# Kernel tuning notes

Hardware: AMD Instinct MI355X
Metric: run time of the kernel (lower is better)

## Reference

```python
import jax, jax.numpy as jnp
import numpy as np

N_USERS = 100000   # n
N_ITEMS = 50000    # m
N_EDGES = 1000000  # observed user-item interactions
D = 64             # embedding dim
ALPHA = 1.0        # Rankformer alpha
CLAMP = 1e-6       # args.rankformer_clamp_value (min clamp on omega norm)


def setup_inputs() -> dict:
    key = jax.random.key(0)
    k1, k2, k3 = jax.random.split(key, 3)
    x = jax.random.normal(k1, (N_USERS + N_ITEMS, D), dtype=jnp.float32)
    u = jax.random.randint(k2, (N_EDGES,), 0, N_USERS, dtype=jnp.int64)
    i = jax.random.randint(k3, (N_EDGES,), 0, N_ITEMS, dtype=jnp.int64)
    return {"x": x, "u": u, "i": i}


def reference(x, u, i):
    seg = jax.ops.segment_sum
    n, m = N_USERS, N_ITEMS
    dt = x.dtype

    # degree of each user; duj = number of non-interacted items
    dui = seg(jnp.ones((u.shape[0],), dt), u, num_segments=n)
    duj = m - dui
    dui = jnp.maximum(dui, 1.0)[:, None]  # [n,1]
    duj = jnp.maximum(duj, 1.0)[:, None]  # [n,1]

    # F.normalize(x): row-wise L2 with eps=1e-12
    xn = x / jnp.maximum(jnp.linalg.norm(x, axis=1, keepdims=True), 1e-12)
    xu, xi = xn[:n], xn[n:]   # normalized user / item features
    vu, vi = x[:n], x[n:]     # raw (value) user / item features

    xi_e = xi[i]              # [E,d] gathered item features per edge
    vi_e = vi[i]
    xui = jnp.sum(xu[u] * xi_e, axis=1, keepdims=True)  # [E,1] edge scores

    sxi = seg(xi_e, u, num_segments=n)          # sum of pos-item x per user
    sxj = jnp.sum(xi, axis=0) - sxi             # rest (neg) sum
    svi = seg(vi_e, u, num_segments=n)
    svj = jnp.sum(vi, axis=0) - svi

    b_pos = jnp.sum(xu * sxi, axis=1, keepdims=True) / dui
    b_neg = jnp.sum(xu * sxj, axis=1, keepdims=True) / duj

    du1 = jnp.sum(xu * sxi, axis=1, keepdims=True) / dui - b_neg + ALPHA
    du2 = -jnp.sum(xu * sxj, axis=1, keepdims=True) / duj + b_pos + ALPHA

    di1 = (jnp.sum(xi * seg((xu / dui)[u], i, num_segments=m), axis=1, keepdims=True)
           + seg(((-b_neg + ALPHA) / dui)[u], i, num_segments=m))
    rest_x = jnp.sum(xu / duj, axis=0)[None, :] - seg((xu / duj)[u], i, num_segments=m)
    rest_b = (jnp.sum((b_pos + ALPHA) / duj, axis=0)[None, :]
              - seg(((b_pos + ALPHA) / duj)[u], i, num_segments=m))
    di2 = -jnp.sum(xi * rest_x, axis=1, keepdims=True) + rest_b

    A = seg(xui * vi_e, u, num_segments=n)      # [n,d]
    # xvi.sum(0): S[a,b] = sum_m vi[m,a]*xi[m,b]  (never materialize [m,d,d])
    S = jnp.einsum('ma,mb->ab', vi, xi)
    zu1 = A / dui - svi * (b_neg - ALPHA) / dui
    zu2 = (xu @ S - A) / duj - svj * (b_pos + ALPHA) / duj

    zi1 = (seg(xui * vu[u] / dui[u], i, num_segments=m)
           - seg((vu * (b_neg - ALPHA) / dui)[u], i, num_segments=m))
    # ((xu/duj) outer vu).sum(0): T[a,b] = sum_n (xu/duj)[n,a]*vu[n,b]
    T = jnp.einsum('na,nb->ab', xu / duj, vu)
    rest_v = (jnp.sum(vu * (b_pos + ALPHA) / duj, axis=0)[None, :]
              - seg((vu * (b_pos + ALPHA) / duj)[u], i, num_segments=m))
    zi2 = xi @ T - seg(xui * (vu / duj)[u], i, num_segments=m) - rest_v

    z = jnp.concatenate([zu1 + zu2, zi1 + zi2], axis=0)          # [n+m,d]
    d1 = jnp.maximum(jnp.concatenate([du1, di1], axis=0), CLAMP)  # [n+m,1]
    d2 = jnp.maximum(jnp.concatenate([du2, di2], axis=0), CLAMP)
    return z / (d1 + d2)
```

## Files before the change

kernel.cpp:

```cpp
#include <hip/hip_runtime.h>

#define NU 100000
#define NI 50000
#define DD 64
#define ALPHA_C 1.0f
#define EPS_CLAMP 1e-6f

__device__ __forceinline__ float rsum16(float v) {
  v += __shfl_xor(v, 1, 64);
  v += __shfl_xor(v, 2, 64);
  v += __shfl_xor(v, 4, 64);
  v += __shfl_xor(v, 8, 64);
  return v;
}
__device__ __forceinline__ float xgrp2(float v) {
  v += __shfl_xor(v, 16, 64);
  v += __shfl_xor(v, 32, 64);
  return v;
}
__device__ __forceinline__ float wsum(float v) { return xgrp2(rsum16(v)); }

__global__ void k_norm_sums(const float* __restrict__ x, float* __restrict__ inv_norm,
                            float* __restrict__ sum_xi, float* __restrict__ sum_vi) {
  __shared__ float sx_s[DD], sv_s[DD];
  if (threadIdx.x < DD) { sx_s[threadIdx.x] = 0.f; sv_s[threadIdx.x] = 0.f; }
  __syncthreads();
  int lane = threadIdx.x & 63;
  int g = lane >> 4, c = lane & 15;
  int wid = blockIdx.x * 4 + (threadIdx.x >> 6);
  int nw  = gridDim.x * 4;
  float sx0=0,sx1=0,sx2=0,sx3=0, sv0=0,sv1=0,sv2=0,sv3=0;
  for (int rb = wid * 4; rb < NU + NI; rb += nw * 4) {
    int r = rb + g;
    const float4 v4 = *(const float4*)(x + (size_t)r * DD + 4 * c);
    float p = v4.x*v4.x + v4.y*v4.y + v4.z*v4.z + v4.w*v4.w;
    p = rsum16(p);
    float inv = 1.0f / fmaxf(sqrtf(p), 1e-12f);
    if (c == 0) inv_norm[r] = inv;
    float fi = (r >= NU) ? 1.f : 0.f;
    float fx = fi * inv;
    sv0 += fi*v4.x; sv1 += fi*v4.y; sv2 += fi*v4.z; sv3 += fi*v4.w;
    sx0 += fx*v4.x; sx1 += fx*v4.y; sx2 += fx*v4.z; sx3 += fx*v4.w;
  }
  atomicAdd(&sx_s[4*c+0], sx0); atomicAdd(&sx_s[4*c+1], sx1);
  atomicAdd(&sx_s[4*c+2], sx2); atomicAdd(&sx_s[4*c+3], sx3);
  atomicAdd(&sv_s[4*c+0], sv0); atomicAdd(&sv_s[4*c+1], sv1);
  atomicAdd(&sv_s[4*c+2], sv2); atomicAdd(&sv_s[4*c+3], sv3);
  __syncthreads();
  if (threadIdx.x < DD) {
    atomicAdd(&sum_xi[threadIdx.x], sx_s[threadIdx.x]);
    atomicAdd(&sum_vi[threadIdx.x], sv_s[threadIdx.x]);
  }
}

__global__ void k_count2(const int* __restrict__ u, const int* __restrict__ it,
                         int* __restrict__ du, int* __restrict__ di,
                         int* __restrict__ ru_, int* __restrict__ ri_, int E) {
  int t = blockIdx.x * blockDim.x + threadIdx.x;
  int stride = gridDim.x * blockDim.x;
  for (int e = t; e < E; e += stride) {
    ru_[e] = atomicAdd(&du[u[e]], 1);
    ri_[e] = atomicAdd(&di[it[e]], 1);
  }
}

__global__ void k_scan2(const int* __restrict__ cnt0, int n0, int* __restrict__ off0,
                        const int* __restrict__ cnt1, int n1, int* __restrict__ off1) {
  const int* cnt = blockIdx.x ? cnt1 : cnt0;
  int n          = blockIdx.x ? n1   : n0;
  int* off       = blockIdx.x ? off1 : off0;
  __shared__ int wsum_s[16];
  __shared__ int carry_s;
  int t = threadIdx.x, lane = t & 63, wv = t >> 6;
  if (t == 0) carry_s = 0;
  __syncthreads();
  for (int base = 0; base < n; base += 1024 * 8) {
    int v[8];
    int s = 0;
    int i0 = base + t * 8;
#pragma unroll
    for (int k = 0; k < 8; ++k) {
      int idx = i0 + k;
      v[k] = (idx < n) ? cnt[idx] : 0;
      s += v[k];
    }
    int incl = s;
#pragma unroll
    for (int d = 1; d < 64; d <<= 1) {
      int t2 = __shfl_up(incl, d, 64);
      if (lane >= d) incl += t2;
    }
    if (lane == 63) wsum_s[wv] = incl;
    __syncthreads();
    int woff = 0, total = 0;
#pragma unroll
    for (int w = 0; w < 16; ++w) {
      int ws_v = wsum_s[w];
      woff += (w < wv) ? ws_v : 0;
      total += ws_v;
    }
    int excl = carry_s + woff + incl - s;
#pragma unroll
    for (int k = 0; k < 8; ++k) {
      int idx = i0 + k;
      if (idx < n) off[idx] = excl;
      excl += v[k];
    }
    __syncthreads();
    if (t == 0) carry_s += total;
    __syncthreads();
  }
  if (t == 0) off[n] = carry_s;
}

__global__ void k_scatter3(const int* __restrict__ u, const int* __restrict__ it,
                           const int* __restrict__ ru_, const int* __restrict__ ri_,
                           const int* __restrict__ uoff, const int* __restrict__ ioff, int E,
                           int* __restrict__ uev, unsigned long long* __restrict__ iue) {
  int t = blockIdx.x * blockDim.x + threadIdx.x;
  int stride = gridDim.x * blockDim.x;
  for (int e = t; e < E; e += stride) {
    int uu = u[e], ii = it[e];
    int pu = uoff[uu] + ru_[e];
    int pi = ioff[ii] + ri_[e];
    __builtin_nontemporal_store(ii, &uev[pu]);
    unsigned long long packed = (unsigned long long)(unsigned)uu |
                                ((unsigned long long)(unsigned)pu << 32);
    __builtin_nontemporal_store(packed, &iue[pi]);
  }
}

#define GRID_OUT 256
#define GS_OUT 85
#define OCH 32
__global__ void k_outer4(const float* __restrict__ x, const float* __restrict__ inv_norm,
                         const int* __restrict__ du, float* __restrict__ part) {
  __shared__ float rows_s[OCH * DD];
  __shared__ float w_s[OCH];
  bool isT = (int)blockIdx.x >= GS_OUT;
  int bloc = isT ? (int)blockIdx.x - GS_OUT : (int)blockIdx.x;
  int nb   = isT ? (GRID_OUT - GS_OUT) : GS_OUT;
  int nrows = isT ? NU : NI;
  int row0  = isT ? 0 : NU;
  int t = threadIdx.x;
  int a0 = (t >> 4) << 2;
  int b0 = (t & 15) << 2;
  float acc[4][4];
#pragma unroll
  for (int i = 0; i < 4; ++i)
#pragma unroll
    for (int j = 0; j < 4; ++j) acc[i][j] = 0.f;
  int nch = (nrows + OCH - 1) / OCH;
  int limit = row0 + nrows;
  for (int ch = bloc; ch < nch; ch += nb) {
    int rbase = row0 + ch * OCH;
    __syncthreads();
    {
      const float4* src = (const float4*)(x + (size_t)rbase * DD);
      float4* dst = (float4*)rows_s;
      int r1 = rbase + (t >> 4);
      dst[t] = (r1 < limit) ? src[t] : make_float4(0.f, 0.f, 0.f, 0.f);
      int r2 = rbase + ((t + 256) >> 4);
      dst[t + 256] = (r2 < limit) ? src[t + 256] : make_float4(0.f, 0.f, 0.f, 0.f);
      if (t < OCH) {
        int r = rbase + t;
        float w = 0.f;
        if (r < limit) {
          w = inv_norm[r];
          if (isT) w /= fmaxf((float)NI - (float)du[r], 1.0f);
        }
        w_s[t] = w;
      }
    }
    __syncthreads();
#pragma unroll 8
    for (int r = 0; r < OCH; ++r) {
      float w = w_s[r];
      const float4 av = *(const float4*)(rows_s + r * DD + a0);
      const float4 bv = *(const float4*)(rows_s + r * DD + b0);
      float wa0 = av.x * w, wa1 = av.y * w, wa2 = av.z * w, wa3 = av.w * w;
      acc[0][0] += wa0 * bv.x; acc[0][1] += wa0 * bv.y; acc[0][2] += wa0 * bv.z; acc[0][3] += wa0 * bv.w;
      acc[1][0] += wa1 * bv.x; acc[1][1] += wa1 * bv.y; acc[1][2] += wa1 * bv.z; acc[1][3] += wa1 * bv.w;
      acc[2][0] += wa2 * bv.x; acc[2][1] += wa2 * bv.y; acc[2][2] += wa2 * bv.z; acc[2][3] += wa2 * bv.w;
      acc[3][0] += wa3 * bv.x; acc[3][1] += wa3 * bv.y; acc[3][2] += wa3 * bv.z; acc[3][3] += wa3 * bv.w;
    }
  }
  float* dst = part + (size_t)blockIdx.x * (DD * DD);
#pragma unroll
  for (int i = 0; i < 4; ++i)
    *(float4*)(dst + (size_t)(a0 + i) * DD + b0) =
        make_float4(acc[i][0], acc[i][1], acc[i][2], acc[i][3]);
}

__global__ void k_redST(const float* __restrict__ part,
                        float* __restrict__ Smat, float* __restrict__ Tmat) {
  int k = blockIdx.x * blockDim.x + threadIdx.x;
  if (k < DD * DD) {
    float s = 0.f;
    for (int b = 0; b < GS_OUT; ++b) s += part[(size_t)b * (DD * DD) + k];
    Smat[k] = s;
  } else {
    int kk = k - DD * DD;
    float s = 0.f;
    for (int b = GS_OUT; b < GRID_OUT; ++b) s += part[(size_t)b * (DD * DD) + kk];
    Tmat[kk] = s;
  }
}

__global__ void k_matvec(const float* __restrict__ x, const float* __restrict__ inv_norm,
                         const float* __restrict__ Smat, const float* __restrict__ Tmat,
                         float* __restrict__ out, int gU) {
  bool isI = (int)blockIdx.x >= gU;
  const float* M = isI ? Tmat : Smat;
  int row0  = isI ? NU : 0;
  int nrows = isI ? NI : NU;
  int bloc  = isI ? (int)blockIdx.x - gU : (int)blockIdx.x;
  int nb    = isI ? (int)gridDim.x - gU : gU;
  int lane = threadIdx.x & 63;
  float m_reg[DD];
#pragma unroll
  for (int a = 0; a < DD; ++a) m_reg[a] = M[a * DD + lane];
  int wid = bloc * (blockDim.x >> 6) + (threadIdx.x >> 6);
  int nw  = nb * (blockDim.x >> 6);
  for (int rr = wid; rr < nrows; rr += nw) {
    int r = row0 + rr;
    float v = x[(size_t)r * DD + lane] * inv_norm[r];
    float a0 = 0.f, a1 = 0.f, a2 = 0.f, a3 = 0.f;
#pragma unroll
    for (int a = 0; a < DD; a += 4) {
      a0 += __shfl(v, a)     * m_reg[a];
      a1 += __shfl(v, a + 1) * m_reg[a + 1];
      a2 += __shfl(v, a + 2) * m_reg[a + 2];
      a3 += __shfl(v, a + 3) * m_reg[a + 3];
    }
    out[(size_t)r * DD + lane] = (a0 + a1) + (a2 + a3);
  }
}

__global__ void k_user4(const float* __restrict__ x, const float* __restrict__ inv_norm,
                        const int* __restrict__ uoff, const int* __restrict__ uev,
                        const float* __restrict__ sum_xi, const float* __restrict__ sum_vi,
                        float* __restrict__ d_raw, float4* __restrict__ usc,
                        float* __restrict__ out,
                        float* __restrict__ Gx, float* __restrict__ Gv, float* __restrict__ Gb) {
  __shared__ float gx_s[DD], gv_s[DD], gb_s;
  if (threadIdx.x < DD) { gx_s[threadIdx.x] = 0.f; gv_s[threadIdx.x] = 0.f; }
  if (threadIdx.x == 0) gb_s = 0.f;
  __syncthreads();
  int lane = threadIdx.x & 63;
  int g = lane >> 4, c = lane & 15;
  float gmask = (g == 0) ? 1.f : 0.f;
  int wid = blockIdx.x * (blockDim.x >> 6) + (threadIdx.x >> 6);
  int nw  = gridDim.x * (blockDim.x >> 6);
  const float4 sx4  = *(const float4*)(sum_xi + 4 * c);
  const float4 svl4 = *(const float4*)(sum_vi + 4 * c);
  float gxa0=0,gxa1=0,gxa2=0,gxa3=0, gva0=0,gva1=0,gva2=0,gva3=0, gb=0.f;
  for (int uu = wid; uu < NU; uu += nw) {
    size_t ru = (size_t)uu * DD;
    int beg = uoff[uu], end2 = uoff[uu + 1];
    int deg = end2 - beg;
    float a1 = 1.0f / fmaxf((float)deg, 1.0f);
    float a2 = 1.0f / fmaxf((float)(NI - deg), 1.0f);
    float invu = inv_norm[uu];
    const float4 v4 = *(const float4*)(x + ru + 4 * c);
    float4 xu4 = make_float4(v4.x*invu, v4.y*invu, v4.z*invu, v4.w*invu);
    float Av0=0,Av1=0,Av2=0,Av3=0, sv0=0,sv1=0,sv2=0,sv3=0;
    float sA = 0.f;
    for (int base = beg; base < end2; base += 64) {
      int nb = end2 - base; if (nb > 64) nb = 64;
      int ii_l = 0; float inv_l = 0.f;
      if (lane < nb) {
        ii_l = uev[base + lane];
        inv_l = inv_norm[NU + ii_l];
      }
      for (int k0 = 0; k0 < nb; k0 += 4) {
        int   ii  = __shfl(ii_l, k0 + g);
        float inj = __shfl(inv_l, k0 + g);
        float f   = (k0 + g < nb) ? 1.f : 0.f;
        const float4 r4 = *(const float4*)(x + (size_t)(NU + ii) * DD + 4 * c);
        float p = xu4.x*r4.x + xu4.y*r4.y + xu4.z*r4.z + xu4.w*r4.w;
        float d = rsum16(p) * inj;
        Av0 += d * r4.x; Av1 += d * r4.y; Av2 += d * r4.z; Av3 += d * r4.w;
        sv0 += f * r4.x; sv1 += f * r4.y; sv2 += f * r4.z; sv3 += f * r4.w;
        sA += d;
        if (c == 0 && k0 + g < nb) d_raw[base + k0 + g] = d;
      }
    }
    sA  = xgrp2(sA);
    Av0 = xgrp2(Av0); Av1 = xgrp2(Av1); Av2 = xgrp2(Av2); Av3 = xgrp2(Av3);
    sv0 = xgrp2(sv0); sv1 = xgrp2(sv1); sv2 = xgrp2(sv2); sv3 = xgrp2(sv3);
    float bp = sA * a1;
    float pbn = xu4.x*sx4.x + xu4.y*sx4.y + xu4.z*sx4.z + xu4.w*sx4.w;
    float bn = (rsum16(pbn) - sA) * a2;
    float s1 = (ALPHA_C - bn) * a1;
    float s2 = (bp + ALPHA_C) * a2;
    if (lane == 0) usc[uu] = make_float4(a1, a2, s1, s2);
    const float4 xs4 = *(const float4*)(out + ru + 4 * c);
    float c12 = s1 + s2, a12 = a1 - a2;
    float rden = 1.0f / (2.0f * fmaxf(bp - bn + ALPHA_C, EPS_CLAMP));
    float o0 = (Av0 * a12 + sv0 * c12 + xs4.x * a2 - svl4.x * s2) * rden;
    float o1 = (Av1 * a12 + sv1 * c12 + xs4.y * a2 - svl4.y * s2) * rden;
    float o2 = (Av2 * a12 + sv2 * c12 + xs4.z * a2 - svl4.z * s2) * rden;
    float o3 = (Av3 * a12 + sv3 * c12 + xs4.w * a2 - svl4.w * s2) * rden;
    if (g == 0) *(float4*)(out + ru + 4 * c) = make_float4(o0, o1, o2, o3);
    float t2 = a2 * gmask, t3 = s2 * gmask;
    gxa0 += t2 * xu4.x; gxa1 += t2 * xu4.y; gxa2 += t2 * xu4.z; gxa3 += t2 * xu4.w;
    gva0 += t3 * v4.x;  gva1 += t3 * v4.y;  gva2 += t3 * v4.z;  gva3 += t3 * v4.w;
    if (lane == 0) gb += s2;
  }
  if (g == 0) {
    atomicAdd(&gx_s[4*c+0], gxa0); atomicAdd(&gx_s[4*c+1], gxa1);
    atomicAdd(&gx_s[4*c+2], gxa2); atomicAdd(&gx_s[4*c+3], gxa3);
    atomicAdd(&gv_s[4*c+0], gva0); atomicAdd(&gv_s[4*c+1], gva1);
    atomicAdd(&gv_s[4*c+2], gva2); atomicAdd(&gv_s[4*c+3], gva3);
  }
  if (lane == 0) atomicAdd(&gb_s, gb);
  __syncthreads();
  if (threadIdx.x < DD) {
    atomicAdd(&Gx[threadIdx.x], gx_s[threadIdx.x]);
    atomicAdd(&Gv[threadIdx.x], gv_s[threadIdx.x]);
  }
  if (threadIdx.x == 0) atomicAdd(Gb, gb_s);
}

__global__ void k_item4(const float* __restrict__ x, const float* __restrict__ inv_norm,
                        const int* __restrict__ ioff, const uint2* __restrict__ iue,
                        const float* __restrict__ d_raw, const float4* __restrict__ usc,
                        const float* __restrict__ Gx, const float* __restrict__ Gv,
                        const float* __restrict__ Gb, float* __restrict__ out) {
  int lane = threadIdx.x & 63;
  int g = lane >> 4, c = lane & 15;
  int wid = blockIdx.x * (blockDim.x >> 6) + (threadIdx.x >> 6);
  int nw  = gridDim.x * (blockDim.x >> 6);
  const float4 Gx4 = *(const float4*)(Gx + 4 * c);
  const float4 Gv4 = *(const float4*)(Gv + 4 * c);
  float gb = *Gb;
  for (int j = wid; j < NI; j += nw) {
    int r = NU + j;
    size_t rr = (size_t)r * DD;
    float invi = inv_norm[r];
    const float4 vi4 = *(const float4*)(x + rr + 4 * c);
    float4 xi4 = make_float4(vi4.x*invi, vi4.y*invi, vi4.z*invi, vi4.w*invi);
    int beg = ioff[j], end2 = ioff[j + 1];
    float W0=0,W1=0,W2=0,W3=0, q1=0.f, q2=0.f;
    for (int base = beg; base < end2; base += 64) {
      int nb = end2 - base; if (nb > 64) nb = 64;
      int uu_l = 0; float glx = 0.f;
      if (lane < nb) {
        uint2 m = iue[base + lane];
        uu_l = (int)m.x;
        float d = d_raw[m.y];
        float4 cc = usc[uu_l];
        float t1 = d * cc.x + cc.z;
        float t2 = d * cc.y - cc.w;
        q1 += t1; q2 += t2;
        glx = t1 - t2;
      }
      for (int k0 = 0; k0 < nb; k0 += 4) {
        int   ua = __shfl(uu_l, k0 + g);
        float ge = __shfl(glx,  k0 + g);
        const float4 r4 = *(const float4*)(x + (size_t)ua * DD + 4 * c);
        W0 += ge * r4.x; W1 += ge * r4.y; W2 += ge * r4.z; W3 += ge * r4.w;
      }
    }
    q1 = wsum(q1); q2 = wsum(q2);
    W0 = xgrp2(W0); W1 = xgrp2(W1); W2 = xgrp2(W2); W3 = xgrp2(W3);
    float pd = xi4.x*Gx4.x + xi4.y*Gx4.y + xi4.z*Gx4.z + xi4.w*Gx4.w;
    float di1 = q1;
    float di2 = -rsum16(pd) + q2 + gb;
    const float4 xt4 = *(const float4*)(out + rr + 4 * c);
    float rden = 1.0f / (fmaxf(di1, EPS_CLAMP) + fmaxf(di2, EPS_CLAMP));
    float o0 = (W0 + xt4.x - Gv4.x) * rden;
    float o1 = (W1 + xt4.y - Gv4.y) * rden;
    float o2 = (W2 + xt4.z - Gv4.z) * rden;
    float o3 = (W3 + xt4.w - Gv4.w) * rden;
    if (g == 0) *(float4*)(out + rr + 4 * c) = make_float4(o0, o1, o2, o3);
  }
}

extern "C" void kernel_launch(void* const* d_in, const int* in_sizes, int n_in,
                              void* d_out, int out_size, void* d_ws, size_t ws_size,
                              hipStream_t stream) {
  const float* x  = (const float*)d_in[0];
  const int*   u  = (const int*)d_in[1];
  const int*   it = (const int*)d_in[2];
  float* out = (float*)d_out;
  const int E = in_sizes[1];

  char* wsb = (char*)d_ws;
  size_t off = 0;
  auto alloc = [&](size_t elems) { void* p = wsb + off; off += elems * 4; return p; };

  int*   du     = (int*)alloc(100016);
  int*   di     = (int*)alloc(50016);
  float* sum_xi = (float*)alloc(64);
  float* sum_vi = (float*)alloc(64);
  float* Gx     = (float*)alloc(64);
  float* Gv     = (float*)alloc(64);
  float* Gb     = (float*)alloc(16);
  size_t zero_bytes = off;

  float* Smat   = (float*)alloc(4096);
  float* Tmat   = (float*)alloc(4096);
  float* part   = (float*)alloc((size_t)GRID_OUT * 4096);
  float*  inv_norm = (float*)alloc(150016);
  int*    uoff     = (int*)alloc(100016);
  int*    ioff     = (int*)alloc(50016);
  int*    ru_      = (int*)alloc(1000000);
  int*    ri_      = (int*)alloc(1000000);
  int*    uev      = (int*)alloc(1000000);
  unsigned long long* iue = (unsigned long long*)alloc(2000000);
  float*  d_raw    = (float*)alloc(1000000);
  float4* usc      = (float4*)alloc(400000);

  hipMemsetAsync(d_ws, 0, zero_bytes, stream);

  k_norm_sums<<<1024, 256, 0, stream>>>(x, inv_norm, sum_xi, sum_vi);
  k_count2<<<2048, 256, 0, stream>>>(u, it, du, di, ru_, ri_, E);
  k_scan2<<<2, 1024, 0, stream>>>(du, NU, uoff, di, NI, ioff);
  k_scatter3<<<4096, 256, 0, stream>>>(u, it, ru_, ri_, uoff, ioff, E, uev, iue);
  k_outer4<<<GRID_OUT, 256, 0, stream>>>(x, inv_norm, du, part);
  k_redST<<<32, 256, 0, stream>>>(part, Smat, Tmat);
  k_matvec<<<1536, 256, 0, stream>>>(x, inv_norm, Smat, Tmat, out, 1024);
  k_user4<<<2048, 256, 0, stream>>>(x, inv_norm, uoff, uev, sum_xi, sum_vi,
                                    d_raw, usc, out, Gx, Gv, Gb);
  k_item4<<<2048, 256, 0, stream>>>(x, inv_norm, ioff, (const uint2*)iue, d_raw, usc,
                                    Gx, Gv, Gb, out);
}
```

Before: 630.5 us.

## Gather fp16 copies of item and user rows in edge kernels; partition scatter writes

The norm pass now also writes half-precision copies of the normalized item rows and the raw user rows. The user and item edge loops gather these 128-byte rows instead of 256-byte fp32 rows, which halves the random gather traffic. Raw item values are rebuilt as normalized fp16 times a stored norm. The scatter kernel is split into 8 block groups, each of which writes only its own slice of output positions, to improve write locality. This costs fp16 rounding error in the edge terms, and every scatter group re-reads all edge inputs.

```diff
diff --git a/kernel.cpp b/kernel.cpp
--- a/kernel.cpp
+++ b/kernel.cpp
@@ -5,6 +5,8 @@
 #define DD 64
 #define ALPHA_C 1.0f
 #define EPS_CLAMP 1e-6f
+
+typedef _Float16 h4 __attribute__((ext_vector_type(4)));
 
 __device__ __forceinline__ float rsum16(float v) {
   v += __shfl_xor(v, 1, 64);
@@ -21,6 +23,8 @@
 __device__ __forceinline__ float wsum(float v) { return xgrp2(rsum16(v)); }
 
 __global__ void k_norm_sums(const float* __restrict__ x, float* __restrict__ inv_norm,
+                            float* __restrict__ nrm, h4* __restrict__ xnih,
+                            h4* __restrict__ vuh,
                             float* __restrict__ sum_xi, float* __restrict__ sum_vi) {
   __shared__ float sx_s[DD], sv_s[DD];
   if (threadIdx.x < DD) { sx_s[threadIdx.x] = 0.f; sv_s[threadIdx.x] = 0.f; }
@@ -35,12 +39,21 @@
     const float4 v4 = *(const float4*)(x + (size_t)r * DD + 4 * c);
     float p = v4.x*v4.x + v4.y*v4.y + v4.z*v4.z + v4.w*v4.w;
     p = rsum16(p);
-    float inv = 1.0f / fmaxf(sqrtf(p), 1e-12f);
+    float nc  = fmaxf(sqrtf(p), 1e-12f);
+    float inv = 1.0f / nc;
     if (c == 0) inv_norm[r] = inv;
-    float fi = (r >= NU) ? 1.f : 0.f;
-    float fx = fi * inv;
-    sv0 += fi*v4.x; sv1 += fi*v4.y; sv2 += fi*v4.z; sv3 += fi*v4.w;
-    sx0 += fx*v4.x; sx1 += fx*v4.y; sx2 += fx*v4.z; sx3 += fx*v4.w;
+    if (r >= NU) {
+      int j = r - NU;
+      if (c == 0) nrm[j] = nc;
+      float xn0 = v4.x*inv, xn1 = v4.y*inv, xn2 = v4.z*inv, xn3 = v4.w*inv;
+      h4 hw = { (_Float16)xn0, (_Float16)xn1, (_Float16)xn2, (_Float16)xn3 };
+      xnih[(size_t)j * 16 + c] = hw;
+      sv0 += v4.x; sv1 += v4.y; sv2 += v4.z; sv3 += v4.w;
+      sx0 += xn0;  sx1 += xn1;  sx2 += xn2;  sx3 += xn3;
+    } else {
+      h4 hw = { (_Float16)v4.x, (_Float16)v4.y, (_Float16)v4.z, (_Float16)v4.w };
+      vuh[(size_t)r * 16 + c] = hw;
+    }
   }
   atomicAdd(&sx_s[4*c+0], sx0); atomicAdd(&sx_s[4*c+1], sx1);
   atomicAdd(&sx_s[4*c+2], sx2); atomicAdd(&sx_s[4*c+3], sx3);
@@ -113,20 +126,26 @@
   if (t == 0) off[n] = carry_s;
 }
 
-__global__ void k_scatter3(const int* __restrict__ u, const int* __restrict__ it,
+__global__ void k_scatter4(const int* __restrict__ u, const int* __restrict__ it,
                            const int* __restrict__ ru_, const int* __restrict__ ri_,
-                           const int* __restrict__ uoff, const int* __restrict__ ioff, int E,
+                           const int* __restrict__ uoff, const int* __restrict__ ioff,
+                           int E, int slice,
                            int* __restrict__ uev, unsigned long long* __restrict__ iue) {
-  int t = blockIdx.x * blockDim.x + threadIdx.x;
-  int stride = gridDim.x * blockDim.x;
+  int part = blockIdx.x & 7;
+  int lo = part * slice, hi = lo + slice;
+  int bloc = (int)blockIdx.x >> 3;
+  int nb = (int)gridDim.x >> 3;
+  int t = bloc * blockDim.x + threadIdx.x;
+  int stride = nb * blockDim.x;
   for (int e = t; e < E; e += stride) {
-    int uu = u[e], ii = it[e];
-    int pu = uoff[uu] + ru_[e];
-    int pi = ioff[ii] + ri_[e];
-    __builtin_nontemporal_store(ii, &uev[pu]);
-    unsigned long long packed = (unsigned long long)(unsigned)uu |
-                                ((unsigned long long)(unsigned)pu << 32);
-    __builtin_nontemporal_store(packed, &iue[pi]);
+    int uu = __builtin_nontemporal_load(&u[e]);
+    int ii = __builtin_nontemporal_load(&it[e]);
+    int pu = uoff[uu] + __builtin_nontemporal_load(&ru_[e]);
+    int pi = ioff[ii] + __builtin_nontemporal_load(&ri_[e]);
+    if (pu >= lo && pu < hi) uev[pu] = ii;
+    if (pi >= lo && pi < hi)
+      iue[pi] = (unsigned long long)(unsigned)uu |
+                ((unsigned long long)(unsigned)pu << 32);
   }
 }
 
@@ -237,7 +256,8 @@
   }
 }
 
-__global__ void k_user4(const float* __restrict__ x, const float* __restrict__ inv_norm,
+__global__ void k_user5(const float* __restrict__ x, const float* __restrict__ inv_norm,
+                        const float* __restrict__ nrm, const h4* __restrict__ xnih,
                         const int* __restrict__ uoff, const int* __restrict__ uev,
                         const float* __restrict__ sum_xi, const float* __restrict__ sum_vi,
                         float* __restrict__ d_raw, float4* __restrict__ usc,
@@ -267,23 +287,25 @@
     float Av0=0,Av1=0,Av2=0,Av3=0, sv0=0,sv1=0,sv2=0,sv3=0;
     float sA = 0.f;
     for (int base = beg; base < end2; base += 64) {
-      int nb = end2 - base; if (nb > 64) nb = 64;
-      int ii_l = 0; float inv_l = 0.f;
-      if (lane < nb) {
+      int nb2 = end2 - base; if (nb2 > 64) nb2 = 64;
+      int ii_l = 0; float nc_l = 0.f;
+      if (lane < nb2) {
         ii_l = uev[base + lane];
-        inv_l = inv_norm[NU + ii_l];
+        nc_l = nrm[ii_l];
       }
-      for (int k0 = 0; k0 < nb; k0 += 4) {
-        int   ii  = __shfl(ii_l, k0 + g);
-        float inj = __shfl(inv_l, k0 + g);
-        float f   = (k0 + g < nb) ? 1.f : 0.f;
-        const float4 r4 = *(const float4*)(x + (size_t)(NU + ii) * DD + 4 * c);
-        float p = xu4.x*r4.x + xu4.y*r4.y + xu4.z*r4.z + xu4.w*r4.w;
-        float d = rsum16(p) * inj;
-        Av0 += d * r4.x; Av1 += d * r4.y; Av2 += d * r4.z; Av3 += d * r4.w;
-        sv0 += f * r4.x; sv1 += f * r4.y; sv2 += f * r4.z; sv3 += f * r4.w;
+      for (int k0 = 0; k0 < nb2; k0 += 4) {
+        int   ii = __shfl(ii_l, k0 + g);
+        float nc = __shfl(nc_l, k0 + g);
+        float f  = (k0 + g < nb2) ? 1.f : 0.f;
+        h4 hv = xnih[(size_t)ii * 16 + c];
+        float r0 = (float)hv.x, r1 = (float)hv.y, r2 = (float)hv.z, r3 = (float)hv.w;
+        float p = xu4.x*r0 + xu4.y*r1 + xu4.z*r2 + xu4.w*r3;
+        float d = f * rsum16(p);
+        float w = d * nc;
+        Av0 += w * r0; Av1 += w * r1; Av2 += w * r2; Av3 += w * r3;
+        sv0 += nc * r0; sv1 += nc * r1; sv2 += nc * r2; sv3 += nc * r3;
         sA += d;
-        if (c == 0 && k0 + g < nb) d_raw[base + k0 + g] = d;
+        if (c == 0 && k0 + g < nb2) d_raw[base + k0 + g] = d;
       }
     }
     sA  = xgrp2(sA);
@@ -323,7 +345,8 @@
   if (threadIdx.x == 0) atomicAdd(Gb, gb_s);
 }
 
-__global__ void k_item4(const float* __restrict__ x, const float* __restrict__ inv_norm,
+__global__ void k_item5(const float* __restrict__ x, const float* __restrict__ inv_norm,
+                        const h4* __restrict__ vuh,
                         const int* __restrict__ ioff, const uint2* __restrict__ iue,
                         const float* __restrict__ d_raw, const float4* __restrict__ usc,
                         const float* __restrict__ Gx, const float* __restrict__ Gv,
@@ -344,9 +367,9 @@
     int beg = ioff[j], end2 = ioff[j + 1];
     float W0=0,W1=0,W2=0,W3=0, q1=0.f, q2=0.f;
     for (int base = beg; base < end2; base += 64) {
-      int nb = end2 - base; if (nb > 64) nb = 64;
+      int nb2 = end2 - base; if (nb2 > 64) nb2 = 64;
       int uu_l = 0; float glx = 0.f;
-      if (lane < nb) {
+      if (lane < nb2) {
         uint2 m = iue[base + lane];
         uu_l = (int)m.x;
         float d = d_raw[m.y];
@@ -356,11 +379,12 @@
         q1 += t1; q2 += t2;
         glx = t1 - t2;
       }
-      for (int k0 = 0; k0 < nb; k0 += 4) {
+      for (int k0 = 0; k0 < nb2; k0 += 4) {
         int   ua = __shfl(uu_l, k0 + g);
         float ge = __shfl(glx,  k0 + g);
-        const float4 r4 = *(const float4*)(x + (size_t)ua * DD + 4 * c);
-        W0 += ge * r4.x; W1 += ge * r4.y; W2 += ge * r4.z; W3 += ge * r4.w;
+        h4 hv = vuh[(size_t)ua * 16 + c];
+        W0 += ge * (float)hv.x; W1 += ge * (float)hv.y;
+        W2 += ge * (float)hv.z; W3 += ge * (float)hv.w;
       }
     }
     q1 = wsum(q1); q2 = wsum(q2);
@@ -404,6 +428,9 @@
   float* Tmat   = (float*)alloc(4096);
   float* part   = (float*)alloc((size_t)GRID_OUT * 4096);
   float*  inv_norm = (float*)alloc(150016);
+  float*  nrm      = (float*)alloc(50016);
+  h4*     xnih     = (h4*)alloc((size_t)NI * 32);
+  h4*     vuh      = (h4*)alloc((size_t)NU * 32);
   int*    uoff     = (int*)alloc(100016);
   int*    ioff     = (int*)alloc(50016);
   int*    ru_      = (int*)alloc(1000000);
@@ -415,15 +442,16 @@
 
   hipMemsetAsync(d_ws, 0, zero_bytes, stream);
 
-  k_norm_sums<<<1024, 256, 0, stream>>>(x, inv_norm, sum_xi, sum_vi);
+  k_norm_sums<<<1024, 256, 0, stream>>>(x, inv_norm, nrm, xnih, vuh, sum_xi, sum_vi);
   k_count2<<<2048, 256, 0, stream>>>(u, it, du, di, ru_, ri_, E);
   k_scan2<<<2, 1024, 0, stream>>>(du, NU, uoff, di, NI, ioff);
-  k_scatter3<<<4096, 256, 0, stream>>>(u, it, ru_, ri_, uoff, ioff, E, uev, iue);
+  k_scatter4<<<4096, 256, 0, stream>>>(u, it, ru_, ri_, uoff, ioff, E, (E + 7) / 8,
+                                       uev, iue);
   k_outer4<<<GRID_OUT, 256, 0, stream>>>(x, inv_norm, du, part);
   k_redST<<<32, 256, 0, stream>>>(part, Smat, Tmat);
   k_matvec<<<1536, 256, 0, stream>>>(x, inv_norm, Smat, Tmat, out, 1024);
-  k_user4<<<2048, 256, 0, stream>>>(x, inv_norm, uoff, uev, sum_xi, sum_vi,
+  k_user5<<<2048, 256, 0, stream>>>(x, inv_norm, nrm, xnih, uoff, uev, sum_xi, sum_vi,
                                     d_raw, usc, out, Gx, Gv, Gb);
-  k_item4<<<2048, 256, 0, stream>>>(x, inv_norm, ioff, (const uint2*)iue, d_raw, usc,
+  k_item5<<<2048, 256, 0, stream>>>(x, inv_norm, vuh, ioff, (const uint2*)iue, d_raw, usc,
                                     Gx, Gv, Gb, out);
 }
```

Result: slower. 684.4 us (+8.5%).
